# Optimization experiments

Hardware: AMD Instinct MI355X
Metric: run time of the kernel (lower is better)

## Reference

```python
import jax, jax.numpy as jnp
import numpy as np

N_NODES = 4_000_000
N_GRAPHS = 4096  # B; fixed for jit (torch derives it from batch.max()+1)
D_FEAT = 8
NUM_CLASSES = 10


def setup_inputs() -> dict:
    key = jax.random.key(0)
    k1, k2, k3, k4, k5 = jax.random.split(key, 5)
    x = jax.random.normal(k1, (N_NODES, D_FEAT), dtype=jnp.float32)
    # sorted segment ids; with ~977 nodes/graph expected, empty segments are vanishingly unlikely
    batch_ids = jnp.sort(jax.random.randint(k2, (N_NODES,), 0, N_GRAPHS, dtype=jnp.int64))
    input_ids = jax.random.randint(k3, (N_GRAPHS, 128), 0, 30522, dtype=jnp.int64)
    attention_mask = jnp.ones((N_GRAPHS, 128), dtype=jnp.int64)
    W = jax.random.normal(k4, (NUM_CLASSES, D_FEAT), dtype=jnp.float32) * (1.0 / np.sqrt(D_FEAT))
    b = jax.random.normal(k5, (NUM_CLASSES,), dtype=jnp.float32) * 0.01
    return {"x": x, "batch_ids": batch_ids, "input_ids": input_ids,
            "attention_mask": attention_mask, "W": W, "b": b}


def reference(x, batch_ids, input_ids, attention_mask, W, b):
    # Segment-mean pooling: replaces the O(B) python loop of masked means
    # with a single-pass scatter-add. input_ids / attention_mask are unused
    # by the original forward (kept for signature fidelity).
    sums = jax.ops.segment_sum(x, batch_ids, num_segments=N_GRAPHS)          # [B, 8]
    counts = jax.ops.segment_sum(jnp.ones((x.shape[0],), x.dtype), batch_ids,
                                 num_segments=N_GRAPHS)                      # [B]
    pooled = sums / counts[:, None]                                          # [B, 8]
    logits = pooled @ W.T + b                                                # [B, 10]
    return logits
```

## Files before the change

kernel.cpp:

```cpp
#include <hip/hip_runtime.h>

constexpr int N_NODES  = 4000000;
constexpr int N_GRAPHS = 4096;
constexpr int D_FEAT   = 8;
constexpr int N_CLS    = 10;

typedef float f32x4 __attribute__((ext_vector_type(4)));
typedef int   i32x4 __attribute__((ext_vector_type(4)));

__global__ __launch_bounds__(256) void scan_bounds(
    const i32x4* __restrict__ ids4, const int* __restrict__ ids,
    int* __restrict__ bounds)
{
    int t = blockIdx.x * blockDim.x + threadIdx.x;
    int base = t * 4;
    if (base >= N_NODES) return;

    i32x4 v = __builtin_nontemporal_load(ids4 + t);
    int prev = (base == 0) ? -1 : ids[base - 1];

    int cur;
    cur = v.x; if (cur != prev) { for (int g = prev + 1; g <= cur; ++g) bounds[g] = base + 0; } prev = cur;
    cur = v.y; if (cur != prev) { for (int g = prev + 1; g <= cur; ++g) bounds[g] = base + 1; } prev = cur;
    cur = v.z; if (cur != prev) { for (int g = prev + 1; g <= cur; ++g) bounds[g] = base + 2; } prev = cur;
    cur = v.w; if (cur != prev) { for (int g = prev + 1; g <= cur; ++g) bounds[g] = base + 3; } prev = cur;

    if (base + 4 >= N_NODES) {
        for (int g = prev + 1; g <= N_GRAPHS; ++g) bounds[g] = N_NODES;
    }
}

__global__ __launch_bounds__(256) void pool_linear(
    const f32x4* __restrict__ xf,
    const int*   __restrict__ bounds,
    const float* __restrict__ W,
    const float* __restrict__ bias,
    float*       __restrict__ out)
{
    int g = blockIdx.x;
    int s = bounds[g];
    int e = bounds[g + 1];
    int len = e - s;
    int nf  = 2 * e;

    f32x4 acc = (f32x4)(0.f);

    for (int i = 2 * s + (int)threadIdx.x; i < nf; i += 512) {
        f32x4 v0 = __builtin_nontemporal_load(xf + i);
        int j = i + 256;
        f32x4 v1;
        bool p = (j < nf);
        if (p) v1 = __builtin_nontemporal_load(xf + j);
        acc += v0;
        if (p) acc += v1;
    }

    #pragma unroll
    for (int off = 32; off >= 2; off >>= 1) {
        acc.x += __shfl_xor(acc.x, off);
        acc.y += __shfl_xor(acc.y, off);
        acc.z += __shfl_xor(acc.z, off);
        acc.w += __shfl_xor(acc.w, off);
    }
    f32x4 other;
    other.x = __shfl_xor(acc.x, 1);
    other.y = __shfl_xor(acc.y, 1);
    other.z = __shfl_xor(acc.z, 1);
    other.w = __shfl_xor(acc.w, 1);

    __shared__ float red[4][D_FEAT];
    __shared__ float mean[D_FEAT];
    int wid  = threadIdx.x >> 6;
    int lane = threadIdx.x & 63;
    if (lane == 0) {
        red[wid][0] = acc.x;   red[wid][1] = acc.y;
        red[wid][2] = acc.z;   red[wid][3] = acc.w;
        red[wid][4] = other.x; red[wid][5] = other.y;
        red[wid][6] = other.z; red[wid][7] = other.w;
    }
    __syncthreads();
    if (threadIdx.x < D_FEAT) {
        float v = red[0][threadIdx.x] + red[1][threadIdx.x]
                + red[2][threadIdx.x] + red[3][threadIdx.x];
        mean[threadIdx.x] = v / (float)len;
    }
    __syncthreads();
    if (threadIdx.x < N_CLS) {
        const float* w = W + (size_t)threadIdx.x * D_FEAT;
        float a = bias[threadIdx.x];
        #pragma unroll
        for (int j = 0; j < D_FEAT; ++j)
            a += mean[j] * w[j];
        out[(size_t)g * N_CLS + threadIdx.x] = a;
    }
}

extern "C" void kernel_launch(void* const* d_in, const int* in_sizes, int n_in,
                              void* d_out, int out_size, void* d_ws, size_t ws_size,
                              hipStream_t stream) {
    const float* x   = (const float*)d_in[0];
    const int*   ids = (const int*)d_in[1];
    const float* W   = (const float*)d_in[4];
    const float* b   = (const float*)d_in[5];
    float*       out = (float*)d_out;

    int* bounds = (int*)d_ws;

    int scan_threads = N_NODES / 4;
    scan_bounds<<<(scan_threads + 255) / 256, 256, 0, stream>>>(
        (const i32x4*)ids, ids, bounds);
    pool_linear<<<N_GRAPHS, 256, 0, stream>>>((const f32x4*)x, bounds, W, b, out);
}
```

Baseline: 29.97 us.

## Fuse segment boundary search into pooling kernel via wave-parallel 32-ary search

Removes the separate kernel that scanned all 4M segment ids to build a bounds array. Each block now finds its own segment start and end with a 32-way parallel search over the sorted ids, each half-wavefront handling one boundary, then pools as before. This drops one launch and a full 16 MB read of the ids. In exchange every block does about five rounds of dependent scattered global loads before it starts streaming x. Note the ids input is int64 in the task but is read as int32, the same as in the old code.

```diff
diff --git a/kernel.cpp b/kernel.cpp
--- a/kernel.cpp
+++ b/kernel.cpp
@@ -6,40 +6,42 @@
 constexpr int N_CLS    = 10;
 
 typedef float f32x4 __attribute__((ext_vector_type(4)));
-typedef int   i32x4 __attribute__((ext_vector_type(4)));
 
-__global__ __launch_bounds__(256) void scan_bounds(
-    const i32x4* __restrict__ ids4, const int* __restrict__ ids,
-    int* __restrict__ bounds)
-{
-    int t = blockIdx.x * blockDim.x + threadIdx.x;
-    int base = t * 4;
-    if (base >= N_NODES) return;
-
-    i32x4 v = __builtin_nontemporal_load(ids4 + t);
-    int prev = (base == 0) ? -1 : ids[base - 1];
-
-    int cur;
-    cur = v.x; if (cur != prev) { for (int g = prev + 1; g <= cur; ++g) bounds[g] = base + 0; } prev = cur;
-    cur = v.y; if (cur != prev) { for (int g = prev + 1; g <= cur; ++g) bounds[g] = base + 1; } prev = cur;
-    cur = v.z; if (cur != prev) { for (int g = prev + 1; g <= cur; ++g) bounds[g] = base + 2; } prev = cur;
-    cur = v.w; if (cur != prev) { for (int g = prev + 1; g <= cur; ++g) bounds[g] = base + 3; } prev = cur;
-
-    if (base + 4 >= N_NODES) {
-        for (int g = prev + 1; g <= N_GRAPHS; ++g) bounds[g] = N_NODES;
-    }
-}
-
-__global__ __launch_bounds__(256) void pool_linear(
-    const f32x4* __restrict__ xf,
-    const int*   __restrict__ bounds,
+__global__ __launch_bounds__(256) void fused_pool_linear(
+    const float* __restrict__ x,
+    const int*   __restrict__ ids,
     const float* __restrict__ W,
     const float* __restrict__ bias,
     float*       __restrict__ out)
 {
-    int g = blockIdx.x;
-    int s = bounds[g];
-    int e = bounds[g + 1];
+    const f32x4* xf = (const f32x4*)x;
+    int g    = blockIdx.x;
+    int lane = threadIdx.x & 63;
+    int half = lane >> 5;
+    int l32  = lane & 31;
+    int target = g + half;
+
+    int lo = 0, hi = N_NODES;
+    while (hi - lo > 32) {
+        int chunk = (hi - lo + 31) >> 5;
+        int pos = lo + l32 * chunk;
+        int v = (pos < hi) ? ids[pos] : 0x7fffffff;
+        unsigned long long m = __ballot(v < target);
+        unsigned int mm = half ? (unsigned int)(m >> 32) : (unsigned int)m;
+        int cnt = __popc(mm);
+        int nlo = cnt ? lo + (cnt - 1) * chunk + 1 : lo;
+        int nhi = (cnt < 32) ? min(lo + cnt * chunk, hi) : hi;
+        lo = nlo; hi = nhi;
+    }
+    {
+        int pos = lo + l32;
+        int v = (pos < hi) ? ids[pos] : 0x7fffffff;
+        unsigned long long m = __ballot(v < target);
+        unsigned int mm = half ? (unsigned int)(m >> 32) : (unsigned int)m;
+        lo += __popc(mm);
+    }
+    int s = __shfl(lo, 0);
+    int e = __shfl(lo, 32);
     int len = e - s;
     int nf  = 2 * e;
 
@@ -70,8 +72,7 @@
 
     __shared__ float red[4][D_FEAT];
     __shared__ float mean[D_FEAT];
-    int wid  = threadIdx.x >> 6;
-    int lane = threadIdx.x & 63;
+    int wid = threadIdx.x >> 6;
     if (lane == 0) {
         red[wid][0] = acc.x;   red[wid][1] = acc.y;
         red[wid][2] = acc.z;   red[wid][3] = acc.w;
@@ -104,10 +105,5 @@
     const float* b   = (const float*)d_in[5];
     float*       out = (float*)d_out;
 
-    int* bounds = (int*)d_ws;
-
-    int scan_threads = N_NODES / 4;
-    scan_bounds<<<(scan_threads + 255) / 256, 256, 0, stream>>>(
-        (const i32x4*)ids, ids, bounds);
-    pool_linear<<<N_GRAPHS, 256, 0, stream>>>((const f32x4*)x, bounds, W, b, out);
+    fused_pool_linear<<<N_GRAPHS, 256, 0, stream>>>(x, ids, W, b, out);
 }
```

Measured after the change: 31.41 us. 1.05x slower.

## Split pooling into fixed-size node chunks with atomic segment accumulation

Applied to the files above, without the earlier changes.

Replaces one-block-per-graph pooling with one wavefront per fixed 512-node chunk. Each chunk walks the segments it overlaps and atomically adds partial sums and counts into a zeroed workspace, and a separate finalize kernel applies the mean and the linear layer. This balances work evenly across waves and adds more in-flight loads per lane via four accumulators. The cost is atomics, one extra kernel launch, and folding the zeroing into the scan kernel, which also drops the nontemporal loads.

```diff
diff --git a/kernel.cpp b/kernel.cpp
--- a/kernel.cpp
+++ b/kernel.cpp
@@ -4,19 +4,31 @@
 constexpr int N_GRAPHS = 4096;
 constexpr int D_FEAT   = 8;
 constexpr int N_CLS    = 10;
+constexpr int CHUNK    = 512;
+constexpr int NCH      = (N_NODES + CHUNK - 1) / CHUNK;
+constexpr int ACC_F32  = N_GRAPHS * D_FEAT + N_GRAPHS;
+constexpr int ZBLK     = ACC_F32 / (256 * 4);
+
+static_assert(ACC_F32 % (256 * 4) == 0, "zero region must tile exactly");
 
 typedef float f32x4 __attribute__((ext_vector_type(4)));
 typedef int   i32x4 __attribute__((ext_vector_type(4)));
 
-__global__ __launch_bounds__(256) void scan_bounds(
+
+__global__ __launch_bounds__(256) void scan_zero(
     const i32x4* __restrict__ ids4, const int* __restrict__ ids,
-    int* __restrict__ bounds)
+    int* __restrict__ bounds, float* __restrict__ acc)
 {
+    if (blockIdx.x < ZBLK) {
+        int z = (blockIdx.x * 256 + threadIdx.x) * 4;
+        *(f32x4*)(acc + z) = (f32x4)(0.f);
+    }
+
     int t = blockIdx.x * blockDim.x + threadIdx.x;
     int base = t * 4;
     if (base >= N_NODES) return;
 
-    i32x4 v = __builtin_nontemporal_load(ids4 + t);
+    i32x4 v = ids4[t];
     int prev = (base == 0) ? -1 : ids[base - 1];
 
     int cur;
@@ -30,69 +42,79 @@
     }
 }
 
-__global__ __launch_bounds__(256) void pool_linear(
+__global__ __launch_bounds__(256, 8) void pool_atomic(
     const f32x4* __restrict__ xf,
+    const int*   __restrict__ ids,
     const int*   __restrict__ bounds,
-    const float* __restrict__ W,
-    const float* __restrict__ bias,
-    float*       __restrict__ out)
+    float*       __restrict__ sums,
+    float*       __restrict__ cnts)
 {
-    int g = blockIdx.x;
-    int s = bounds[g];
-    int e = bounds[g + 1];
-    int len = e - s;
-    int nf  = 2 * e;
+    int w = blockIdx.x * 4 + (threadIdx.x >> 6);
+    if (w >= NCH) return;
+    int lane = threadIdx.x & 63;
 
-    f32x4 acc = (f32x4)(0.f);
+    int c0 = w * CHUNK;
+    int c1 = min(c0 + CHUNK, N_NODES);
+    int g0 = ids[c0];
+    int g1 = ids[c1 - 1];
 
-    for (int i = 2 * s + (int)threadIdx.x; i < nf; i += 512) {
-        f32x4 v0 = __builtin_nontemporal_load(xf + i);
-        int j = i + 256;
-        f32x4 v1;
-        bool p = (j < nf);
-        if (p) v1 = __builtin_nontemporal_load(xf + j);
-        acc += v0;
-        if (p) acc += v1;
+    int p = c0, gcur = g0;
+    while (true) {
+        int pend = (gcur < g1) ? bounds[gcur + 1] : c1;
+        f32x4 a0 = (f32x4)(0.f), a1 = (f32x4)(0.f),
+              a2 = (f32x4)(0.f), a3 = (f32x4)(0.f);
+        int i = 2 * p + lane;
+        int endf = 2 * pend;
+        int full = (endf - 2 * p) >> 8;
+        for (int it = 0; it < full; ++it, i += 256) {
+            a0 += xf[i];
+            a1 += xf[i +  64];
+            a2 += xf[i + 128];
+            a3 += xf[i + 192];
+        }
+        for (; i < endf; i += 64) a0 += xf[i];
+        f32x4 acc = (a0 + a1) + (a2 + a3);
+
+        #pragma unroll
+        for (int off = 32; off >= 2; off >>= 1) {
+            acc.x += __shfl_xor(acc.x, off);
+            acc.y += __shfl_xor(acc.y, off);
+            acc.z += __shfl_xor(acc.z, off);
+            acc.w += __shfl_xor(acc.w, off);
+        }
+        if (lane < 2 && pend > p) {
+            float* s = sums + (size_t)gcur * D_FEAT + lane * 4;
+            atomicAdd(s + 0, acc.x);
+            atomicAdd(s + 1, acc.y);
+            atomicAdd(s + 2, acc.z);
+            atomicAdd(s + 3, acc.w);
+        }
+        if (lane == 0 && pend > p)
+            atomicAdd(cnts + gcur, (float)(pend - p));
+
+        if (pend >= c1) break;
+        p = pend;
+        ++gcur;
     }
+}
 
+__global__ __launch_bounds__(256) void finalize(
+    const float* __restrict__ sums, const float* __restrict__ cnts,
+    const float* __restrict__ W, const float* __restrict__ bias,
+    float* __restrict__ out)
+{
+    int idx = blockIdx.x * blockDim.x + threadIdx.x;
+    if (idx >= N_GRAPHS * N_CLS) return;
+    int g = idx / N_CLS;
+    int c = idx % N_CLS;
+    float inv = 1.0f / cnts[g];
+    const float* s = sums + (size_t)g * D_FEAT;
+    const float* w = W + (size_t)c * D_FEAT;
+    float a = bias[c];
     #pragma unroll
-    for (int off = 32; off >= 2; off >>= 1) {
-        acc.x += __shfl_xor(acc.x, off);
-        acc.y += __shfl_xor(acc.y, off);
-        acc.z += __shfl_xor(acc.z, off);
-        acc.w += __shfl_xor(acc.w, off);
-    }
-    f32x4 other;
-    other.x = __shfl_xor(acc.x, 1);
-    other.y = __shfl_xor(acc.y, 1);
-    other.z = __shfl_xor(acc.z, 1);
-    other.w = __shfl_xor(acc.w, 1);
-
-    __shared__ float red[4][D_FEAT];
-    __shared__ float mean[D_FEAT];
-    int wid  = threadIdx.x >> 6;
-    int lane = threadIdx.x & 63;
-    if (lane == 0) {
-        red[wid][0] = acc.x;   red[wid][1] = acc.y;
-        red[wid][2] = acc.z;   red[wid][3] = acc.w;
-        red[wid][4] = other.x; red[wid][5] = other.y;
-        red[wid][6] = other.z; red[wid][7] = other.w;
-    }
-    __syncthreads();
-    if (threadIdx.x < D_FEAT) {
-        float v = red[0][threadIdx.x] + red[1][threadIdx.x]
-                + red[2][threadIdx.x] + red[3][threadIdx.x];
-        mean[threadIdx.x] = v / (float)len;
-    }
-    __syncthreads();
-    if (threadIdx.x < N_CLS) {
-        const float* w = W + (size_t)threadIdx.x * D_FEAT;
-        float a = bias[threadIdx.x];
-        #pragma unroll
-        for (int j = 0; j < D_FEAT; ++j)
-            a += mean[j] * w[j];
-        out[(size_t)g * N_CLS + threadIdx.x] = a;
-    }
+    for (int k = 0; k < D_FEAT; ++k)
+        a += (s[k] * inv) * w[k];
+    out[idx] = a;
 }
 
 extern "C" void kernel_launch(void* const* d_in, const int* in_sizes, int n_in,
@@ -104,10 +126,18 @@
     const float* b   = (const float*)d_in[5];
     float*       out = (float*)d_out;
 
-    int* bounds = (int*)d_ws;
+    float* sums   = (float*)d_ws;
+    float* cnts   = sums + (size_t)N_GRAPHS * D_FEAT;
+    int*   bounds = (int*)(cnts + N_GRAPHS);
 
-    int scan_threads = N_NODES / 4;
-    scan_bounds<<<(scan_threads + 255) / 256, 256, 0, stream>>>(
-        (const i32x4*)ids, ids, bounds);
-    pool_linear<<<N_GRAPHS, 256, 0, stream>>>((const f32x4*)x, bounds, W, b, out);
+    int scan_blocks = (N_NODES / 4 + 255) / 256;
+    scan_zero<<<scan_blocks, 256, 0, stream>>>(
+        (const i32x4*)ids, ids, bounds, sums);
+
+    int pool_blocks = (NCH + 3) / 4;
+    pool_atomic<<<pool_blocks, 256, 0, stream>>>(
+        (const f32x4*)x, ids, bounds, sums, cnts);
+
+    finalize<<<(N_GRAPHS * N_CLS + 255) / 256, 256, 0, stream>>>(
+        sums, cnts, W, b, out);
 }
```

Result: slower. 33.16 us (+10.7%).
